# Kernel tuning notes

Hardware: AMD Instinct MI355X
Metric: run time of the kernel (lower is better)

Reference implementation:

```python
import jax, jax.numpy as jnp
import numpy as np

NUM_T = 1000
B, N = 16, 2048
M = 8192


def _cosine_alphas_cumprod(T=NUM_T, s=0.008):
    # Faithful to ColdDiffusion.cosine_beta_schedule + cumprod of (1 - betas)
    x = np.linspace(0.0, T, T + 1)
    ac = np.cos((x / T + s) / (1 + s) * np.pi * 0.5) ** 2
    ac = ac / ac[0]
    betas = np.clip(1.0 - ac[1:] / ac[:-1], 0.0001, 0.9999)
    return np.cumprod(1.0 - betas)


def setup_inputs() -> dict:
    key = jax.random.key(0)
    k1, k2, k3 = jax.random.split(key, 3)
    x_start = jax.random.normal(k1, (B, N, 4, 2), dtype=jnp.float32)
    anchors = jax.random.normal(k2, (M, 4, 2), dtype=jnp.float32)
    t = jax.random.randint(k3, (B,), 0, NUM_T)
    ac = _cosine_alphas_cumprod()
    sqrt_alphas_cumprod = jnp.asarray(np.sqrt(ac), dtype=jnp.float32)
    sqrt_one_minus_alphas_cumprod = jnp.asarray(np.sqrt(1.0 - ac), dtype=jnp.float32)
    return {
        "x_start": x_start,
        "anchors": anchors,
        "sqrt_alphas_cumprod": sqrt_alphas_cumprod,
        "sqrt_one_minus_alphas_cumprod": sqrt_one_minus_alphas_cumprod,
        "t": t,
    }


def reference(x_start, anchors, sqrt_alphas_cumprod, sqrt_one_minus_alphas_cumprod, t):
    # q_sample with anchor matching, fully batched (no Python loop over B).
    Bq, Nq = x_start.shape[:2]
    xf = x_start.reshape(Bq, Nq, -1)            # [B,N,8]
    af = anchors.reshape(anchors.shape[0], -1)  # [M,8]
    scores = jnp.einsum('bnd,md->bnm', xf, af) * (-2.0) + jnp.sum(af * af, axis=-1)  # [B,N,M]
    idx = jnp.argmin(scores, axis=-1)           # [B,N]
    matched = anchors[idx]                      # [B,N,4,2] gather
    sa = sqrt_alphas_cumprod[t][:, None, None, None]                 # [B,1,1,1]
    sb = sqrt_one_minus_alphas_cumprod[t][:, None, None, None]       # [B,1,1,1]
    return sa * x_start + sb * matched
```

## Files before the change

### kernel.cpp

```cpp
#include <hip/hip_runtime.h>
#include <stdint.h>

#define B_      16
#define N_      2048
#define M_      8192
#define ROWS    (B_ * N_)
#define D_      8

#define QUARTERS 8
#define APQ     (M_ / QUARTERS)
#define CHUNK   256
#define NCHUNK  (APQ / CHUNK)
#define TPC     (CHUNK / 16)
#define WROWS   64
#define BROWS_A 256
#define GRIDX   (ROWS / BROWS_A)

#define OFF_NH  0
#define OFF_NM  4096
#define OFF_NL  8192
#define OFF_HN  12288
#define CHUNK_BYTES 13312
#define SMEM_BYTES 36864


typedef short bf16x8 __attribute__((ext_vector_type(8)));
typedef float f32x4  __attribute__((ext_vector_type(4)));

__device__ __forceinline__ unsigned short f2bf(float f) {
    unsigned u = __float_as_uint(f);
    u += 0x7FFFu + ((u >> 16) & 1u);
    return (unsigned short)(u >> 16);
}
__device__ __forceinline__ float bf2f(unsigned short h) {
    return __uint_as_float(((unsigned)h) << 16);
}

__global__ __launch_bounds__(256) void prep_kernel(
    const float* __restrict__ anchors, char* __restrict__ pk)
{
    const int a = blockIdx.x * 256 + threadIdx.x;
    const float4* pa = (const float4*)(anchors + (size_t)a * D_);
    const float4 g0 = pa[0], g1 = pa[1];
    float nv[8] = {-g0.x, -g0.y, -g0.z, -g0.w, -g1.x, -g1.y, -g1.z, -g1.w};
    bf16x8 vh, vm, vl;
    #pragma unroll
    for (int k = 0; k < 8; ++k) {
        unsigned short h = f2bf(nv[k]);
        float r1 = nv[k] - bf2f(h);
        unsigned short m = f2bf(r1);
        float r2 = r1 - bf2f(m);
        unsigned short l = f2bf(r2);
        vh[k] = (short)h; vm[k] = (short)m; vl[k] = (short)l;
    }
    char* base = pk + (size_t)(a >> 8) * CHUNK_BYTES;
    const int i = a & 255;
    *(bf16x8*)(base + OFF_NH + i * 16) = vh;
    *(bf16x8*)(base + OFF_NM + i * 16) = vm;
    *(bf16x8*)(base + OFF_NL + i * 16) = vl;
    float nr = nv[0] * nv[0];
    #pragma unroll
    for (int k = 1; k < 8; ++k) nr = fmaf(nv[k], nv[k], nr);
    *(float*)(base + OFF_HN + i * 4) = 0.5f * nr;
}

__global__ __launch_bounds__(256)
__attribute__((amdgpu_waves_per_eu(4, 4)))
void argmin_mfma_kernel(
    const float* __restrict__ x,
    const char*  __restrict__ pk,
    float* __restrict__ wsv,
    int*   __restrict__ wsi)
{
    __shared__ __align__(16) char smem[SMEM_BYTES];

    const int tid  = threadIdx.x;
    const int wave = tid >> 6;
    const int lane = tid & 63;
    const int n    = lane & 15;
    const int kb   = lane >> 4;

    const int quarter = blockIdx.y;
    const int abase   = quarter * APQ;
    const int wrow0   = blockIdx.x * BROWS_A + wave * WROWS;

    const char* srcq = pk + (size_t)quarter * NCHUNK * CHUNK_BYTES;

    {
        char* bufw = smem;
        #pragma unroll
        for (int sg = 0; sg < 3; ++sg) {
            const int seg = (wave + sg * 4) * 1024;
            __builtin_amdgcn_global_load_lds(srcq + seg + lane * 16,
                                             bufw + seg, 16, 0, 0);
        }
        if (wave == 0)
            __builtin_amdgcn_global_load_lds(srcq + 12288 + lane * 16,
                                             bufw + 12288, 16, 0, 0);
    }

    bf16x8 A1[4], A2[4];
    #pragma unroll
    for (int rt = 0; rt < 4; ++rt) {
        const int row = wrow0 + rt * 16 + n;
        const float4* px = (const float4*)(x + (size_t)row * D_);
        const float4 lo = px[0], hi = px[1];
        const float v[8] = {lo.x, lo.y, lo.z, lo.w, hi.x, hi.y, hi.z, hi.w};
        const bool odd = (kb & 1);
        const bool is2 = (kb == 2);
        #pragma unroll
        for (int k = 0; k < 8; ++k) {
            unsigned short xh = f2bf(v[k]);
            float r1 = v[k] - bf2f(xh);
            unsigned short xm = f2bf(r1);
            float r2 = r1 - bf2f(xm);
            unsigned short xl = f2bf(r2);
            A1[rt][k] = (short)(odd ? xm : xh);
            A2[rt][k] = (short)(odd ? xl : (is2 ? xm : xh));
        }
    }

    const int o1 = ((kb < 2) ? OFF_NH : OFF_NM) + n * 16;
    const int o2 = ((kb == 1) ? OFF_NH : (kb == 3) ? OFF_NM : OFF_NL) + n * 16;
    const int oh = OFF_HN + n * 4;

    float best[4][4];
    int   bidx[4][4];
    #pragma unroll
    for (int rt = 0; rt < 4; ++rt)
        #pragma unroll
        for (int q = 0; q < 4; ++q) { best[rt][q] = 3.4e38f; bidx[rt][q] = 0; }

    int idxv = abase + n;

    __syncthreads();

    #pragma unroll 1
    for (int c = 0; c < NCHUNK; ++c) {
        const char* bufr = smem + (c & 1) * CHUNK_BYTES;

        if (c < NCHUNK - 1) {
            char* bufw = smem + ((c & 1) ^ 1) * CHUNK_BYTES;
            const char* g = srcq + (size_t)(c + 1) * CHUNK_BYTES;
            #pragma unroll
            for (int sg = 0; sg < 3; ++sg) {
                const int seg = (wave + sg * 4) * 1024;
                __builtin_amdgcn_global_load_lds(g + seg + lane * 16,
                                                 bufw + seg, 16, 0, 0);
            }
            if (wave == 0)
                __builtin_amdgcn_global_load_lds(g + 12288 + lane * 16,
                                                 bufw + 12288, 16, 0, 0);
        }

        #pragma unroll 2
        for (int tt = 0; tt < TPC; ++tt) {
            const bf16x8 b1 = *(const bf16x8*)(bufr + o1 + tt * 256);
            const bf16x8 b2 = *(const bf16x8*)(bufr + o2 + tt * 256);
            const float  hn = *(const float*)(bufr + oh + tt * 64);
            const f32x4 cvec = {hn, hn, hn, hn};
            #pragma unroll
            for (int rt = 0; rt < 4; ++rt) {
                f32x4 acc = __builtin_amdgcn_mfma_f32_16x16x32_bf16(A1[rt], b1, cvec, 0, 0, 0);
                acc = __builtin_amdgcn_mfma_f32_16x16x32_bf16(A2[rt], b2, acc, 0, 0, 0);
                #pragma unroll
                for (int q = 0; q < 4; ++q) {
                    const bool lt = acc[q] < best[rt][q];
                    best[rt][q] = lt ? acc[q] : best[rt][q];
                    bidx[rt][q] = lt ? idxv   : bidx[rt][q];
                }
            }
            idxv += 16;
        }

        __syncthreads();
    }

    #pragma unroll
    for (int rt = 0; rt < 4; ++rt) {
        #pragma unroll
        for (int q = 0; q < 4; ++q) {
            float bv = best[rt][q]; int bi = bidx[rt][q];
            #pragma unroll
            for (int m = 1; m < 16; m <<= 1) {
                const float ov = __shfl_xor(bv, m);
                const int   oi = __shfl_xor(bi, m);
                const bool take = (ov < bv) || (ov == bv && oi < bi);
                bv = take ? ov : bv;
                bi = take ? oi : bi;
            }
            if ((lane & 15) == 0) {
                const int row = wrow0 + rt * 16 + (lane >> 4) * 4 + q;
                wsv[(size_t)quarter * ROWS + row] = bv;
                wsi[(size_t)quarter * ROWS + row] = bi;
            }
        }
    }
}

__global__ __launch_bounds__(256) void combine_kernel(
    const float* __restrict__ x,
    const float* __restrict__ anchors,
    const float* __restrict__ sa_tab,
    const float* __restrict__ sb_tab,
    const int*   __restrict__ t,
    const float* __restrict__ wsv,
    const int*   __restrict__ wsi,
    float* __restrict__ out)
{
    const int row = blockIdx.x * 256 + threadIdx.x;

    float bv = wsv[row];
    int   bi = wsi[row];
    #pragma unroll
    for (int qq = 1; qq < QUARTERS; ++qq) {
        const float v = wsv[(size_t)qq * ROWS + row];
        const int   i = wsi[(size_t)qq * ROWS + row];
        const bool take = (v < bv) || (v == bv && i < bi);
        bv = take ? v : bv;
        bi = take ? i : bi;
    }

    const int b  = row >> 11;
    const int tb = t[b];
    const float sa = sa_tab[tb];
    const float sb = sb_tab[tb];

    const float4* px = (const float4*)(x + (size_t)row * D_);
    const float4 xlo = px[0], xhi = px[1];
    const float4* pa = (const float4*)(anchors + (size_t)bi * D_);
    const float4 a0 = pa[0], a1 = pa[1];

    float4 o0, o1;
    o0.x = fmaf(sa, xlo.x, sb * a0.x);
    o0.y = fmaf(sa, xlo.y, sb * a0.y);
    o0.z = fmaf(sa, xlo.z, sb * a0.z);
    o0.w = fmaf(sa, xlo.w, sb * a0.w);
    o1.x = fmaf(sa, xhi.x, sb * a1.x);
    o1.y = fmaf(sa, xhi.y, sb * a1.y);
    o1.z = fmaf(sa, xhi.z, sb * a1.z);
    o1.w = fmaf(sa, xhi.w, sb * a1.w);

    float4* po = (float4*)(out + (size_t)row * D_);
    po[0] = o0;
    po[1] = o1;
}

extern "C" void kernel_launch(void* const* d_in, const int* in_sizes, int n_in,
                              void* d_out, int out_size, void* d_ws, size_t ws_size,
                              hipStream_t stream) {
    const float* x       = (const float*)d_in[0];
    const float* anchors = (const float*)d_in[1];
    const float* sa_tab  = (const float*)d_in[2];
    const float* sb_tab  = (const float*)d_in[3];
    const int*   t       = (const int*)d_in[4];
    float* out = (float*)d_out;

    float* wsv = (float*)d_ws;
    int*   wsi = (int*)((char*)d_ws + (size_t)1024 * 1024);
    char*  pk  = (char*)d_ws + (size_t)2048 * 1024;

    prep_kernel<<<M_ / 256, 256, 0, stream>>>(anchors, pk);

    dim3 gridA(GRIDX, QUARTERS);
    argmin_mfma_kernel<<<gridA, 256, 0, stream>>>(x, pk, wsv, wsi);

    combine_kernel<<<ROWS / 256, 256, 0, stream>>>(
        x, anchors, sa_tab, sb_tab, t, wsv, wsi, out);
}
```

Before: 112.8 us.

## Track only min values in MFMA pass and rescan winning segment for index

The MFMA argmin loop now keeps only the running minimum value per row, using fminf instead of a compare-select on both value and index. This removes the index registers and the select instructions from the hot loop. A new rescan kernel picks, for each row, the anchor segment that holds the global minimum. Blocks assigned to that segment load its anchors into LDS and recompute exact fp32 distances over those 1024 anchors to recover the index, then write the blended output. The extra cost is the rescan work. Near-ties between segments may also resolve differently from before, because the segment choice uses the approximate MFMA values while the index comes from fp32.

```diff
diff --git a/kernel.cpp b/kernel.cpp
--- a/kernel.cpp
+++ b/kernel.cpp
@@ -69,8 +69,7 @@
 void argmin_mfma_kernel(
     const float* __restrict__ x,
     const char*  __restrict__ pk,
-    float* __restrict__ wsv,
-    int*   __restrict__ wsi)
+    float* __restrict__ wsv)
 {
     __shared__ __align__(16) char smem[SMEM_BYTES];
 
@@ -81,7 +80,6 @@
     const int kb   = lane >> 4;
 
     const int quarter = blockIdx.y;
-    const int abase   = quarter * APQ;
     const int wrow0   = blockIdx.x * BROWS_A + wave * WROWS;
 
     const char* srcq = pk + (size_t)quarter * NCHUNK * CHUNK_BYTES;
@@ -125,13 +123,10 @@
     const int oh = OFF_HN + n * 4;
 
     float best[4][4];
-    int   bidx[4][4];
     #pragma unroll
     for (int rt = 0; rt < 4; ++rt)
         #pragma unroll
-        for (int q = 0; q < 4; ++q) { best[rt][q] = 3.4e38f; bidx[rt][q] = 0; }
-
-    int idxv = abase + n;
+        for (int q = 0; q < 4; ++q) best[rt][q] = 3.4e38f;
 
     __syncthreads();
 
@@ -164,13 +159,9 @@
                 f32x4 acc = __builtin_amdgcn_mfma_f32_16x16x32_bf16(A1[rt], b1, cvec, 0, 0, 0);
                 acc = __builtin_amdgcn_mfma_f32_16x16x32_bf16(A2[rt], b2, acc, 0, 0, 0);
                 #pragma unroll
-                for (int q = 0; q < 4; ++q) {
-                    const bool lt = acc[q] < best[rt][q];
-                    best[rt][q] = lt ? acc[q] : best[rt][q];
-                    bidx[rt][q] = lt ? idxv   : bidx[rt][q];
-                }
+                for (int q = 0; q < 4; ++q)
+                    best[rt][q] = fminf(best[rt][q], acc[q]);
             }
-            idxv += 16;
         }
 
         __syncthreads();
@@ -180,70 +171,139 @@
     for (int rt = 0; rt < 4; ++rt) {
         #pragma unroll
         for (int q = 0; q < 4; ++q) {
-            float bv = best[rt][q]; int bi = bidx[rt][q];
+            float bv = best[rt][q];
             #pragma unroll
-            for (int m = 1; m < 16; m <<= 1) {
-                const float ov = __shfl_xor(bv, m);
-                const int   oi = __shfl_xor(bi, m);
-                const bool take = (ov < bv) || (ov == bv && oi < bi);
-                bv = take ? ov : bv;
-                bi = take ? oi : bi;
-            }
+            for (int m = 1; m < 16; m <<= 1)
+                bv = fminf(bv, __shfl_xor(bv, m));
             if ((lane & 15) == 0) {
                 const int row = wrow0 + rt * 16 + (lane >> 4) * 4 + q;
                 wsv[(size_t)quarter * ROWS + row] = bv;
-                wsi[(size_t)quarter * ROWS + row] = bi;
             }
         }
     }
 }
 
-__global__ __launch_bounds__(256) void combine_kernel(
+#define BQ 256
+__global__ __launch_bounds__(256) void rescan_kernel(
     const float* __restrict__ x,
     const float* __restrict__ anchors,
     const float* __restrict__ sa_tab,
     const float* __restrict__ sb_tab,
     const int*   __restrict__ t,
     const float* __restrict__ wsv,
-    const int*   __restrict__ wsi,
     float* __restrict__ out)
 {
-    const int row = blockIdx.x * 256 + threadIdx.x;
-
-    float bv = wsv[row];
-    int   bi = wsi[row];
-    #pragma unroll
-    for (int qq = 1; qq < QUARTERS; ++qq) {
-        const float v = wsv[(size_t)qq * ROWS + row];
-        const int   i = wsi[(size_t)qq * ROWS + row];
-        const bool take = (v < bv) || (v == bv && i < bi);
-        bv = take ? v : bv;
-        bi = take ? i : bi;
-    }
-
-    const int b  = row >> 11;
-    const int tb = t[b];
-    const float sa = sa_tab[tb];
-    const float sb = sb_tab[tb];
-
-    const float4* px = (const float4*)(x + (size_t)row * D_);
-    const float4 xlo = px[0], xhi = px[1];
-    const float4* pa = (const float4*)(anchors + (size_t)bi * D_);
-    const float4 a0 = pa[0], a1 = pa[1];
-
-    float4 o0, o1;
-    o0.x = fmaf(sa, xlo.x, sb * a0.x);
-    o0.y = fmaf(sa, xlo.y, sb * a0.y);
-    o0.z = fmaf(sa, xlo.z, sb * a0.z);
-    o0.w = fmaf(sa, xlo.w, sb * a0.w);
-    o1.x = fmaf(sa, xhi.x, sb * a1.x);
-    o1.y = fmaf(sa, xhi.y, sb * a1.y);
-    o1.z = fmaf(sa, xhi.z, sb * a1.z);
-    o1.w = fmaf(sa, xhi.w, sb * a1.w);
-
-    float4* po = (float4*)(out + (size_t)row * D_);
-    po[0] = o0;
-    po[1] = o1;
+    __shared__ __align__(16) float sAq[APQ * D_];
+    __shared__ unsigned short rowlist[BQ];
+    __shared__ int cnt;
+
+    const int tid  = threadIdx.x;
+    const int q    = blockIdx.y;
+    const int row0 = blockIdx.x * BQ;
+
+    if (tid == 0) cnt = 0;
+    __syncthreads();
+
+    {
+        const int row = row0 + tid;
+        float bv = wsv[row];
+        int   bq = 0;
+        #pragma unroll
+        for (int qq = 1; qq < QUARTERS; ++qq) {
+            const float v = wsv[(size_t)qq * ROWS + row];
+            const bool c = v < bv;
+            bv = c ? v : bv;
+            bq = c ? qq : bq;
+        }
+        if (bq == q) {
+            const int p = atomicAdd(&cnt, 1);
+            rowlist[p] = (unsigned short)tid;
+        }
+    }
+    __syncthreads();
+    const int nrows = cnt;
+    if (nrows == 0) return;
+
+    {
+        const float4* gA = (const float4*)(anchors + (size_t)q * APQ * D_);
+        float4* b = (float4*)sAq;
+        #pragma unroll
+        for (int i = 0; i < 8; ++i)
+            b[tid + i * 256] = gA[tid + i * 256];
+    }
+    __syncthreads();
+
+    const int g   = tid & 7;
+    const int grp = tid >> 3;
+    for (int i = grp; i < nrows; i += 32) {
+        const int row = row0 + rowlist[i];
+        const float4* px = (const float4*)(x + (size_t)row * D_);
+        const float4 xlo = px[0], xhi = px[1];
+        const float X0 = xlo.x, X1 = xlo.y, X2 = xlo.z, X3 = xlo.w;
+        const float X4 = xhi.x, X5 = xhi.y, X6 = xhi.z, X7 = xhi.w;
+
+        float bs = 3.4e38f;
+        int   bl = 0x7FFFFFFF;
+        #pragma unroll 4
+        for (int j = 0; j < APQ / 8; ++j) {
+            const int al = j * 8 + g;
+            const float4* pa = (const float4*)(&sAq[al * D_]);
+            const float4 g0 = pa[0], g1 = pa[1];
+            const float na0 = -g0.x, na1 = -g0.y, na2 = -g0.z, na3 = -g0.w;
+            const float na4 = -g1.x, na5 = -g1.y, na6 = -g1.z, na7 = -g1.w;
+            float nr = na0 * na0;
+            nr = fmaf(na1, na1, nr);
+            nr = fmaf(na2, na2, nr);
+            nr = fmaf(na3, na3, nr);
+            nr = fmaf(na4, na4, nr);
+            nr = fmaf(na5, na5, nr);
+            nr = fmaf(na6, na6, nr);
+            nr = fmaf(na7, na7, nr);
+            const float hn = 0.5f * nr;
+            float s = fmaf(X0, na0, hn);
+            s = fmaf(X1, na1, s);
+            s = fmaf(X2, na2, s);
+            s = fmaf(X3, na3, s);
+            s = fmaf(X4, na4, s);
+            s = fmaf(X5, na5, s);
+            s = fmaf(X6, na6, s);
+            s = fmaf(X7, na7, s);
+            const bool lt = s < bs;
+            bs = lt ? s  : bs;
+            bl = lt ? al : bl;
+        }
+        #pragma unroll
+        for (int m = 1; m < 8; m <<= 1) {
+            const float ov = __shfl_xor(bs, m);
+            const int   ol = __shfl_xor(bl, m);
+            const bool take = (ov < bs) || (ov == bs && ol < bl);
+            bs = take ? ov : bs;
+            bl = take ? ol : bl;
+        }
+
+        if (g == 0) {
+            const int bi = q * APQ + bl;
+            const int b  = row >> 11;
+            const int tb = t[b];
+            const float sa = sa_tab[tb];
+            const float sb = sb_tab[tb];
+            const float4* pa = (const float4*)(&sAq[bl * D_]);
+            const float4 a0 = pa[0], a1 = pa[1];
+            (void)bi;
+            float4 o0, o1;
+            o0.x = fmaf(sa, xlo.x, sb * a0.x);
+            o0.y = fmaf(sa, xlo.y, sb * a0.y);
+            o0.z = fmaf(sa, xlo.z, sb * a0.z);
+            o0.w = fmaf(sa, xlo.w, sb * a0.w);
+            o1.x = fmaf(sa, xhi.x, sb * a1.x);
+            o1.y = fmaf(sa, xhi.y, sb * a1.y);
+            o1.z = fmaf(sa, xhi.z, sb * a1.z);
+            o1.w = fmaf(sa, xhi.w, sb * a1.w);
+            float4* po = (float4*)(out + (size_t)row * D_);
+            po[0] = o0;
+            po[1] = o1;
+        }
+    }
 }
 
 extern "C" void kernel_launch(void* const* d_in, const int* in_sizes, int n_in,
@@ -257,14 +317,14 @@
     float* out = (float*)d_out;
 
     float* wsv = (float*)d_ws;
-    int*   wsi = (int*)((char*)d_ws + (size_t)1024 * 1024);
-    char*  pk  = (char*)d_ws + (size_t)2048 * 1024;
+    char*  pk  = (char*)d_ws + (size_t)1024 * 1024;
 
     prep_kernel<<<M_ / 256, 256, 0, stream>>>(anchors, pk);
 
     dim3 gridA(GRIDX, QUARTERS);
-    argmin_mfma_kernel<<<gridA, 256, 0, stream>>>(x, pk, wsv, wsi);
-
-    combine_kernel<<<ROWS / 256, 256, 0, stream>>>(
-        x, anchors, sa_tab, sb_tab, t, wsv, wsi, out);
-}
+    argmin_mfma_kernel<<<gridA, 256, 0, stream>>>(x, pk, wsv);
+
+    dim3 gridB(ROWS / BQ, QUARTERS);
+    rescan_kernel<<<gridB, 256, 0, stream>>>(
+        x, anchors, sa_tab, sb_tab, t, wsv, out);
+}
```

Result: slower. 116.0 us (+2.9%).
